# Kernel tuning notes

Measured on AMD Instinct MI355X. Metric: run time of the kernel, lower is better.

## Reference

```python
import jax, jax.numpy as jnp
import numpy as np

EPS = 1e-8
MARGIN = 0.2
LAMBDA_SM_LSE = 6.0   # i2t attention smooth (opt.lambda_softmax_lse)
LAMBDA_SM_AVG = 9.0   # t2i attention smooth (opt.lambda_softmax_avg)
LAMBDA_LSE = 6.0      # LogSumExp aggregation temperature
NEG = -1e9


def _l2norm(x, axis):
    return x / (jnp.sqrt(jnp.sum(x * x, axis=axis, keepdims=True)) + EPS)


def _cos(a, b):
    # cosine over last axis, torch-style: w12 / clamp(|a||b|, eps)
    w12 = jnp.sum(a * b, axis=-1)
    w1 = jnp.sqrt(jnp.sum(a * a, axis=-1))
    w2 = jnp.sqrt(jnp.sum(b * b, axis=-1))
    return w12 / jnp.maximum(w1 * w2, EPS)


def _forward(im, s, s_l):
    B, R, D = im.shape
    W = s.shape[1]
    wmask = jnp.arange(W)[None, :] < s_l[:, None]          # (Bc, W) valid words
    s = s * wmask[:, :, None]                              # emulate ragged slice s[j,:len_j]

    # ---------------- i2t: query=image regions, context=caption words ----------
    # attn[i,j,w,r] = <s[j,w], im[i,r]>
    A = jnp.einsum('jwd,ird->ijwr', s, im)
    A = jax.nn.leaky_relu(A, 0.1)
    A = _l2norm(A, axis=3)                                 # clipped_l2norm over regions
    logits = jnp.swapaxes(A, 2, 3) * LAMBDA_SM_LSE         # (i,j,r,w), softmax over words
    logits = jnp.where(wmask[None, :, None, :], logits, NEG)
    attn_i2t = jax.nn.softmax(logits, axis=-1)
    wc_t = jnp.einsum('ijrw,jwd->ijrd', attn_i2t, s)       # weighted caption ctx per region
    sim1 = _cos(im[:, None, :, :], wc_t)                   # (i,j,r)
    score1 = jnp.log(jnp.sum(jnp.exp(LAMBDA_LSE * sim1), axis=2)) / LAMBDA_LSE  # (i,j)
    attn_t_full = jnp.mean(wc_t, axis=2)                   # (i,j,d)
    idx = jnp.arange(B)
    attn_t = attn_t_full[idx, idx]                         # (B,d) diagonal

    # ---------------- t2i: query=caption words, context=image regions ----------
    # attn[i,j,r,w] = <im[i,r], s[j,w]>
    Bm = jnp.einsum('ird,jwd->ijrw', im, s)
    Bm = jax.nn.leaky_relu(Bm, 0.1)
    Bm = Bm * wmask[None, :, None, :]                      # padded-word cols excluded from norm
    Bm = _l2norm(Bm, axis=3)                               # clipped_l2norm over words
    logits2 = jnp.swapaxes(Bm, 2, 3) * LAMBDA_SM_AVG       # (i,j,w,r), softmax over regions
    attn_t2i = jax.nn.softmax(logits2, axis=-1)
    wc_i = jnp.einsum('ijwr,ird->ijwd', attn_t2i, im)      # weighted image ctx per word
    sim2 = _cos(s[None, :, :, :], wc_i)                    # (i,j,w)
    e2 = jnp.where(wmask[None, :, :], jnp.exp(LAMBDA_LSE * sim2), 0.0)
    score2 = jnp.log(jnp.sum(e2, axis=2)) / LAMBDA_LSE     # masked LogSumExp over words
    wsum = jnp.sum(wc_i * wmask[None, :, :, None], axis=2)
    attn_i_full = wsum / s_l[None, :, None].astype(wc_i.dtype)  # masked mean over words
    attn_i = attn_i_full[idx, idx]                         # (B,d)

    # ---------------- hinge loss over (B,B) score matrix -----------------------
    scores = 0.5 * (score1 + score2)
    diag = jnp.diagonal(scores)
    cost_s = jnp.maximum(MARGIN + scores - diag[:, None], 0.0)
    cost_im = jnp.maximum(MARGIN + scores - diag[None, :], 0.0)
    eye = jnp.eye(B, dtype=bool)
    cost_s = jnp.where(eye, 0.0, cost_s)
    cost_im = jnp.where(eye, 0.0, cost_im)
    # max_violation=True
    loss = jnp.sum(jnp.max(cost_s, axis=1)) + jnp.sum(jnp.max(cost_im, axis=0))
    return loss, attn_t, attn_i


def setup_inputs() -> dict:
    key = jax.random.key(0)
    k1, k2, k3 = jax.random.split(key, 3)
    B, R, W, D = 64, 36, 40, 1024
    im = jax.random.normal(k1, (B, R, D), dtype=jnp.float32)
    s = jax.random.normal(k2, (B, W, D), dtype=jnp.float32)
    s_l = jax.random.randint(k3, (B,), 10, W + 1)
    return {"im": im, "s": s, "s_l": s_l}


def reference(im, s, s_l):
    return _forward(im, s, s_l)
```

## Files before the change

kernel.cpp:

```cpp
#include <hip/hip_runtime.h>
#include <math.h>

#define Bn 64
#define Rr 36
#define Ww 40
#define Dd 1024
#define GM 2304
#define GN 2560
#define NCONV 4864
#define PAD 72
#define SBP 64
#define TSZ 1440
#define EPSf 1e-8f

typedef unsigned short u16;
typedef __attribute__((ext_vector_type(8))) short bf16x8;
typedef __attribute__((ext_vector_type(4))) float f32x4;

struct alignas(8) U16x4 { u16 x, y, z, w; };

__device__ inline u16 f2bf(float x) {
    unsigned int u = __float_as_uint(x);
    u += 0x7FFFu + ((u >> 16) & 1u);
    return (u16)(u >> 16);
}
__device__ inline float bf2f(u16 h) {
    return __uint_as_float(((unsigned int)h) << 16);
}

__device__ __forceinline__ void gl_lds16(const u16* g, u16* l) {
    __builtin_amdgcn_global_load_lds(
        (const __attribute__((address_space(1))) void*)g,
        (__attribute__((address_space(3))) void*)l, 16, 0, 0);
}

__global__ __launch_bounds__(256) void prep_kernel(const float* __restrict__ im,
                                                   const float* __restrict__ s,
                                                   const int* __restrict__ s_l,
                                                   u16* __restrict__ Ab,
                                                   u16* __restrict__ Bb,
                                                   u16* __restrict__ SSb,
                                                   u16* __restrict__ IIb,
                                                   float* __restrict__ SSd,
                                                   float* __restrict__ IId) {
    __shared__ float red[3][64][37];
    int b = blockIdx.x, t = threadIdx.x;
    if (b < NCONV) {
        const int nA4 = GM * Dd / 4;
        int idx = b * 256 + t;
        if (idx < nA4) {
            float4 v = *(const float4*)(im + (size_t)idx * 4);
            U16x4 o = {f2bf(v.x), f2bf(v.y), f2bf(v.z), f2bf(v.w)};
            *(U16x4*)(Ab + (size_t)idx * 4) = o;
        } else {
            int i2 = idx - nA4;
            int f = i2 * 4;
            int row = f >> 10;
            int j = row / Ww, w = row - j * Ww;
            U16x4 o = {0, 0, 0, 0};
            if (w < s_l[j]) {
                float4 v = *(const float4*)(s + (size_t)f);
                o.x = f2bf(v.x); o.y = f2bf(v.y); o.z = f2bf(v.z); o.w = f2bf(v.w);
            }
            *(U16x4*)(Bb + (size_t)i2 * 4) = o;
        }
        return;
    }
    int gb = b - NCONV;
    bool isS = gb < Bn;
    int idx = isS ? gb : gb - Bn;
    int n = isS ? Ww : Rr;
    const float* basef = isS ? (s + (size_t)idx * Ww * Dd) : (im + (size_t)idx * Rr * Dd);
    u16* outb = isS ? (SSb + (size_t)idx * 48 * SBP) : (IIb + (size_t)idx * 48 * SBP);
    float* outd = isS ? (SSd + (size_t)idx * Ww) : (IId + (size_t)idx * Rr);
    int lane = t & 63, wid = t >> 6;
    int frow = lane & 15, fk = (lane >> 4) * 8;

    f32x4 acc[3][3];
    for (int m = 0; m < 3; ++m)
        for (int p = 0; p < 3; ++p) acc[m][p] = (f32x4){0.f, 0.f, 0.f, 0.f};

    for (int ks = 0; ks < 8; ++ks) {
        int k0 = wid * 256 + ks * 32 + fk;
        bf16x8 f[3];
        for (int m = 0; m < 3; ++m) {
            int rr = m * 16 + frow;
            if (rr >= n) rr = n - 1;
            const float* p = basef + (size_t)rr * Dd + k0;
            float4 v0 = *(const float4*)p;
            float4 v1 = *(const float4*)(p + 4);
            bf16x8 fv;
            fv[0] = (short)f2bf(v0.x); fv[1] = (short)f2bf(v0.y);
            fv[2] = (short)f2bf(v0.z); fv[3] = (short)f2bf(v0.w);
            fv[4] = (short)f2bf(v1.x); fv[5] = (short)f2bf(v1.y);
            fv[6] = (short)f2bf(v1.z); fv[7] = (short)f2bf(v1.w);
            f[m] = fv;
        }
        for (int m = 0; m < 3; ++m)
            for (int p = 0; p < 3; ++p)
                acc[m][p] = __builtin_amdgcn_mfma_f32_16x16x32_bf16(f[m], f[p], acc[m][p], 0, 0, 0);
    }
    if (wid) {
        for (int m = 0; m < 3; ++m)
            for (int p = 0; p < 3; ++p)
                for (int q = 0; q < 4; ++q)
                    red[wid - 1][lane][(m * 3 + p) * 4 + q] = acc[m][p][q];
    }
    __syncthreads();
    if (wid == 0) {
        for (int wv = 0; wv < 3; ++wv)
            for (int m = 0; m < 3; ++m)
                for (int p = 0; p < 3; ++p)
                    for (int q = 0; q < 4; ++q)
                        acc[m][p][q] += red[wv][lane][(m * 3 + p) * 4 + q];
        int crow = (lane >> 4) * 4, ccol = lane & 15;
        for (int m = 0; m < 3; ++m)
            for (int p = 0; p < 3; ++p)
                for (int q = 0; q < 4; ++q) {
                    int row = m * 16 + crow + q;
                    int col = p * 16 + ccol;
                    float v = acc[m][p][q];
                    outb[row * SBP + col] = f2bf(v);
                    if (row == col && row < n) outd[row] = v;
                }
    }
}

__global__ __launch_bounds__(256) void gemm_mfma_kernel(const u16* __restrict__ Ab,
                                                        const u16* __restrict__ Bb,
                                                        u16* __restrict__ Gt) {
    __shared__ __align__(16) u16 As[3][64][64];
    __shared__ __align__(16) u16 Bs[3][128][64];
    int bn = blockIdx.x;
    int bm = blockIdx.y;
    int t = threadIdx.x;
    int lane = t & 63, wid = t >> 6;
    int wr = wid >> 1, wc = wid & 1;

    int lrow8 = lane >> 3;
    int sslot = (lane & 7) ^ lrow8;
    const u16* ga = Ab + ((size_t)(bm * 64 + wid * 16) + lrow8) * Dd + sslot * 8;
    const u16* gb = Bb + ((size_t)(bn * 128 + wid * 32) + lrow8) * Dd + sslot * 8;

    f32x4 acc[2][4];
    for (int m = 0; m < 2; ++m)
        for (int n = 0; n < 4; ++n) acc[m][n] = (f32x4){0.f, 0.f, 0.f, 0.f};

    int frow = lane & 15;
    int cgr = lane >> 4;

#define STAGE(BI, KK) do { \
        gl_lds16(ga + (KK), &As[BI][wid * 16][0]); \
        gl_lds16(ga + (size_t)8 * Dd + (KK), &As[BI][wid * 16 + 8][0]); \
        gl_lds16(gb + (KK), &Bs[BI][wid * 32][0]); \
        gl_lds16(gb + (size_t)8 * Dd + (KK), &Bs[BI][wid * 32 + 8][0]); \
        gl_lds16(gb + (size_t)16 * Dd + (KK), &Bs[BI][wid * 32 + 16][0]); \
        gl_lds16(gb + (size_t)24 * Dd + (KK), &Bs[BI][wid * 32 + 24][0]); \
    } while (0)

    STAGE(0, 0);
    STAGE(1, 64);
#pragma unroll
    for (int s = 0; s < 16; ++s) {
        if (s < 15) asm volatile("s_waitcnt vmcnt(6)" ::: "memory");
        else        asm volatile("s_waitcnt vmcnt(0)" ::: "memory");
        __builtin_amdgcn_sched_barrier(0);
        __builtin_amdgcn_s_barrier();
        __builtin_amdgcn_sched_barrier(0);
        const int cur = s % 3;
        bf16x8 af[2][2], bf[4][2];
#pragma unroll
        for (int m = 0; m < 2; ++m) {
            int row = wr * 32 + m * 16 + frow;
#pragma unroll
            for (int ks = 0; ks < 2; ++ks) {
                int slot = (ks * 4 + cgr) ^ (row & 7);
                af[m][ks] = *(const bf16x8*)&As[cur][row][slot * 8];
            }
        }
#pragma unroll
        for (int n = 0; n < 4; ++n) {
            int row = wc * 64 + n * 16 + frow;
#pragma unroll
            for (int ks = 0; ks < 2; ++ks) {
                int slot = (ks * 4 + cgr) ^ (row & 7);
                bf[n][ks] = *(const bf16x8*)&Bs[cur][row][slot * 8];
            }
        }
        if (s + 2 < 16) STAGE((s + 2) % 3, (s + 2) * 64);
#pragma unroll
        for (int ks = 0; ks < 2; ++ks)
#pragma unroll
            for (int m = 0; m < 2; ++m)
#pragma unroll
                for (int n = 0; n < 4; ++n)
                    acc[m][n] = __builtin_amdgcn_mfma_f32_16x16x32_bf16(af[m][ks], bf[n][ks], acc[m][n], 0, 0, 0);
        asm volatile("s_waitcnt lgkmcnt(0)" ::: "memory");
        __builtin_amdgcn_sched_barrier(0);
    }
#undef STAGE

    int crow0 = bm * 64 + wr * 32 + (lane >> 4) * 4;
    int ccol0 = bn * 128 + wc * 64 + (lane & 15);
    int tjv[4], wv[4];
#pragma unroll
    for (int n = 0; n < 4; ++n) {
        int col = ccol0 + n * 16;
        tjv[n] = col / 40;
        wv[n] = col - tjv[n] * 40;
    }
    for (int m = 0; m < 2; ++m)
        for (int q = 0; q < 4; ++q) {
            int row = crow0 + m * 16 + q;
            int ti = row / 36, r2 = row - ti * 36;
            u16* dstbase = Gt + (size_t)ti * Bn * TSZ + (size_t)r2 * 40;
            for (int n = 0; n < 4; ++n)
                dstbase[(size_t)tjv[n] * TSZ + wv[n]] = f2bf(acc[m][n][q]);
        }
}

__device__ __forceinline__ void quad_mfma(const u16* att, const u16* M,
                                          float* qout, int nq, int lane) {
    int c = lane & 15, g4 = lane >> 4;
    f32x4 acc[3][3];
#pragma unroll
    for (int m = 0; m < 3; ++m)
#pragma unroll
        for (int p = 0; p < 3; ++p) acc[m][p] = (f32x4){0.f, 0.f, 0.f, 0.f};
#pragma unroll
    for (int ks = 0; ks < 2; ++ks) {
        bf16x8 fa[3], fb[3];
#pragma unroll
        for (int m = 0; m < 3; ++m)
            fa[m] = *(const bf16x8*)&att[(m * 16 + c) * PAD + g4 * 8 + ks * 32];
#pragma unroll
        for (int p = 0; p < 3; ++p)
            fb[p] = *(const bf16x8*)(M + (size_t)(p * 16 + c) * SBP + g4 * 8 + ks * 32);
#pragma unroll
        for (int m = 0; m < 3; ++m)
#pragma unroll
            for (int p = 0; p < 3; ++p)
                acc[m][p] = __builtin_amdgcn_mfma_f32_16x16x32_bf16(fa[m], fb[p], acc[m][p], 0, 0, 0);
    }
#pragma unroll
    for (int m = 0; m < 3; ++m)
#pragma unroll
        for (int q = 0; q < 4; ++q) {
            int row = m * 16 + g4 * 4 + q;
            float sp = 0.f;
#pragma unroll
            for (int p = 0; p < 3; ++p)
                sp += acc[m][p][q] * bf2f(att[row * PAD + p * 16 + c]);
            sp += __shfl_xor(sp, 1);
            sp += __shfl_xor(sp, 2);
            sp += __shfl_xor(sp, 4);
            sp += __shfl_xor(sp, 8);
            if (c == 0 && row < nq) qout[row] = sp;
        }
}

__global__ __launch_bounds__(128) void pair_kernel(const u16* __restrict__ Gt,
                                                   const u16* __restrict__ SSb,
                                                   const u16* __restrict__ IIb,
                                                   const float* __restrict__ SSd,
                                                   const float* __restrict__ IId,
                                                   const int* __restrict__ s_l,
                                                   float* __restrict__ score1,
                                                   float* __restrict__ score2,
                                                   float* __restrict__ dAp,
                                                   float* __restrict__ dBp) {
    int j = blockIdx.x, i = blockIdx.y;
    int t = threadIdx.x, lane = t & 63, wid = t >> 6;
    __shared__ __align__(16) u16 glb[Rr * 44];
    __shared__ __align__(16) u16 attA[48 * PAD];
    __shared__ __align__(16) u16 attB[48 * PAD];
    __shared__ float invA[Ww], invB[Rr], sA[Rr], sB[Ww], qA[Rr], qB[Ww];
    int L = s_l[j];

    {
        uint* za = (uint*)attA;
        uint* zb = (uint*)attB;
#pragma unroll
        for (int k = 0; k < 14; ++k) {
            int idx = t + k * 128;
            if (idx < 48 * PAD / 2) { za[idx] = 0; zb[idx] = 0; }
        }
        const u16* gt = Gt + (size_t)(i * Bn + j) * TSZ;
        for (int c = t; c < 180; c += 128) {
            int r = c / 5, q = c - (c / 5) * 5;
            uint4 v = *(const uint4*)(gt + c * 8);
            *(uint2*)&glb[r * 44 + q * 8] = make_uint2(v.x, v.y);
            *(uint2*)&glb[r * 44 + q * 8 + 4] = make_uint2(v.z, v.w);
        }
    }
    float iid = 0.f, ssd = 0.f;
    if (wid == 0 && lane < Rr) iid = IId[i * Rr + lane];
    if (wid == 1 && lane < Ww) ssd = SSd[j * Ww + lane];
    __syncthreads();

    if (wid == 0 && lane < Rr) {
        float sum = 0.f;
#pragma unroll 8
        for (int w = 0; w < Ww; ++w) {
            float x = bf2f(glb[lane * 44 + w]);
            x = x < 0.f ? 0.1f * x : x;
            sum += x * x;
        }
        invB[lane] = 9.f / (sqrtf(sum) + EPSf);
    }
    if (wid == 1 && lane < Ww) {
        float sum = 0.f;
#pragma unroll 6
        for (int r = 0; r < Rr; ++r) {
            float x = bf2f(glb[r * 44 + lane]);
            x = x < 0.f ? 0.1f * x : x;
            sum += x * x;
        }
        invA[lane] = 6.f / (sqrtf(sum) + EPSf);
    }
    __syncthreads();

    float dot = 0.f, myinv = 0.f;
    if (wid == 0 && lane < Rr) {
        float ssum = 0.f;
#pragma unroll 8
        for (int w = 0; w < Ww; ++w) {
            float e = 0.f;
            if (w < L) {
                float gx = bf2f(glb[lane * 44 + w]);
                float x = gx < 0.f ? 0.1f * gx : gx;
                e = __expf(x * invA[w]);
                dot += e * gx;
            }
            attA[lane * PAD + w] = f2bf(e);
            ssum += e;
        }
        myinv = 1.f / ssum;
        dot *= myinv;
        sA[lane] = myinv;
    }
    if (wid == 1 && lane < Ww) {
        float ssum = 0.f;
#pragma unroll 6
        for (int r = 0; r < Rr; ++r) {
            float gx = bf2f(glb[r * 44 + lane]);
            float x = gx < 0.f ? 0.1f * gx : gx;
            float e = __expf(x * invB[r]);
            dot += e * gx;
            attB[lane * PAD + r] = f2bf(e);
            ssum += e;
        }
        myinv = 1.f / ssum;
        dot *= myinv;
        sB[lane] = myinv;
    }
    __syncthreads();

    if (wid == 0)
        quad_mfma(attA, SSb + (size_t)j * 48 * SBP, qA, Rr, lane);
    else
        quad_mfma(attB, IIb + (size_t)i * 48 * SBP, qB, Ww, lane);

    if (wid == 0) {
        float e1 = 0.f;
        if (lane < Rr) {
            float q = qA[lane] * myinv * myinv;
            float s1 = dot / fmaxf(sqrtf(iid) * sqrtf(fmaxf(q, 0.f)), EPSf);
            e1 = __expf(6.f * s1);
        }
#pragma unroll
        for (int off = 1; off < 64; off <<= 1) e1 += __shfl_xor(e1, off);
        if (lane == 0) score1[i * Bn + j] = __logf(e1) * (1.f / 6.f);
    } else {
        float e2 = 0.f;
        if (lane < Ww) {
            float q = qB[lane] * myinv * myinv;
            float s2 = dot / fmaxf(sqrtf(ssd) * sqrtf(fmaxf(q, 0.f)), EPSf);
            e2 = (lane < L) ? __expf(6.f * s2) : 0.f;
        }
#pragma unroll
        for (int off = 1; off < 64; off <<= 1) e2 += __shfl_xor(e2, off);
        if (lane == 0) score2[i * Bn + j] = __logf(e2) * (1.f / 6.f);
    }

    if (i == j) {
        __syncthreads();
        if (wid == 1 && lane < Ww) {
            float sum = 0.f;
#pragma unroll 6
            for (int r = 0; r < Rr; ++r) sum += bf2f(attA[r * PAD + lane]) * sA[r];
            dAp[i * Ww + lane] = sum * (1.f / (float)Rr);
        }
        if (wid == 0 && lane < Rr) {
            float sum = 0.f;
            for (int w = 0; w < L; ++w) sum += bf2f(attB[w * PAD + lane]) * sB[w];
            dBp[i * Rr + lane] = sum / (float)L;
        }
    }
}

__global__ __launch_bounds__(128) void diag_out_kernel(const u16* __restrict__ Ab,
                                                       const u16* __restrict__ Bb,
                                                       const int* __restrict__ s_l,
                                                       const float* __restrict__ dA,
                                                       const float* __restrict__ dB,
                                                       const float* __restrict__ score1,
                                                       const float* __restrict__ score2,
                                                       float* __restrict__ out) {
    int t = threadIdx.x;
    int bi = blockIdx.x;
    if (bi == Bn) {
        __shared__ float sc[Bn][Bn + 1];
        for (int idx = t; idx < Bn * Bn; idx += 128)
            sc[idx >> 6][idx & 63] = 0.5f * (score1[idx] + score2[idx]);
        __syncthreads();
        if (t < 64) {
            float dt = sc[t][t];
            float rowmax = 0.f, colmax = 0.f;
            for (int k = 0; k < Bn; ++k) {
                if (k != t) {
                    rowmax = fmaxf(rowmax, 0.2f + sc[t][k] - dt);
                    colmax = fmaxf(colmax, 0.2f + sc[k][t] - dt);
                }
            }
            float v = rowmax + colmax;
            for (int off = 32; off; off >>= 1) v += __shfl_down(v, off);
            if (t == 0) out[0] = v;
        }
        return;
    }
    int i = bi;
    int L = s_l[i];
    __shared__ float aw[Ww], br[Rr];
    if (t < Ww) aw[t] = dA[i * Ww + t];
    if (t >= 64 && t < 64 + Rr) br[t - 64] = dB[i * Rr + (t - 64)];
    __syncthreads();
    int d0 = t * 8;
    const u16* BbI = Bb + (size_t)i * Ww * Dd + d0;
    const u16* AbI = Ab + (size_t)i * Rr * Dd + d0;
    float a1[8], a2[8];
#pragma unroll
    for (int k = 0; k < 8; ++k) { a1[k] = 0.f; a2[k] = 0.f; }
    for (int w = 0; w < L; ++w) {
        bf16x8 v = *(const bf16x8*)(BbI + (size_t)w * Dd);
        float c = aw[w];
#pragma unroll
        for (int k = 0; k < 8; ++k) a1[k] += c * bf2f((u16)v[k]);
    }
#pragma unroll 6
    for (int r = 0; r < Rr; ++r) {
        bf16x8 v = *(const bf16x8*)(AbI + (size_t)r * Dd);
        float c = br[r];
#pragma unroll
        for (int k = 0; k < 8; ++k) a2[k] += c * bf2f((u16)v[k]);
    }
    float* o1 = out + 1 + (size_t)i * Dd + d0;
    float* o2 = out + 1 + (size_t)Bn * Dd + (size_t)i * Dd + d0;
#pragma unroll
    for (int k = 0; k < 8; ++k) { o1[k] = a1[k]; o2[k] = a2[k]; }
}

extern "C" void kernel_launch(void* const* d_in, const int* in_sizes, int n_in,
                              void* d_out, int out_size, void* d_ws, size_t ws_size,
                              hipStream_t stream) {
    const float* im = (const float*)d_in[0];
    const float* s = (const float*)d_in[1];
    const int* s_l = (const int*)d_in[2];
    float* out = (float*)d_out;

    u16* Ab = (u16*)d_ws;
    u16* Bb = Ab + (size_t)GM * Dd;
    u16* Gt = Bb + (size_t)GN * Dd;
    u16* SSb = Gt + (size_t)GM * GN;
    u16* IIb = SSb + (size_t)Bn * 48 * SBP;
    float* SSd = (float*)(IIb + (size_t)Bn * 48 * SBP);
    float* IId = SSd + (size_t)Bn * Ww;
    float* score1 = IId + (size_t)Bn * Rr;
    float* score2 = score1 + Bn * Bn;
    float* dA = score2 + Bn * Bn;
    float* dB = dA + Bn * Ww;

    prep_kernel<<<NCONV + 2 * Bn, 256, 0, stream>>>(im, s, s_l, Ab, Bb, SSb, IIb, SSd, IId);

    dim3 ggrid(GN / 128, GM / 64);
    gemm_mfma_kernel<<<ggrid, 256, 0, stream>>>(Ab, Bb, Gt);

    dim3 pgrid(Bn, Bn);
    pair_kernel<<<pgrid, 128, 0, stream>>>(Gt, SSb, IIb, SSd, IId, s_l,
                                           score1, score2, dA, dB);

    diag_out_kernel<<<Bn + 1, 128, 0, stream>>>(Ab, Bb, s_l, dA, dB, score1, score2, out);
}
```

Measured before the change: 78.94 us.

## Move Gram blocks into GEMM grid, fuse diag output into pair kernel, simplify pipeline

The per-batch Gram matrices (SS, II) are now computed by extra blocks appended to the GEMM grid, reading the already-converted bf16 buffers instead of reconverting fp32, so the prep kernel becomes a pure conversion pass. The diagonal attention output (attn_t, attn_i) is computed inside the pair kernel's diagonal blocks, which removes the separate diag kernel and the dA/dB round-trip. The loss reduction moves to a tiny single-block kernel. The GEMM main loop drops from a 3-stage hand-scheduled pipeline with explicit waitcnts to a simpler 2-stage loop with __syncthreads, which may reduce load/compute overlap. Diagonal pair blocks also take on extra serial work.

```diff
diff --git a/kernel.cpp b/kernel.cpp
--- a/kernel.cpp
+++ b/kernel.cpp
@@ -34,107 +34,101 @@
         (__attribute__((address_space(3))) void*)l, 16, 0, 0);
 }
 
-__global__ __launch_bounds__(256) void prep_kernel(const float* __restrict__ im,
-                                                   const float* __restrict__ s,
-                                                   const int* __restrict__ s_l,
-                                                   u16* __restrict__ Ab,
-                                                   u16* __restrict__ Bb,
-                                                   u16* __restrict__ SSb,
-                                                   u16* __restrict__ IIb,
-                                                   float* __restrict__ SSd,
-                                                   float* __restrict__ IId) {
-    __shared__ float red[3][64][37];
-    int b = blockIdx.x, t = threadIdx.x;
-    if (b < NCONV) {
-        const int nA4 = GM * Dd / 4;
-        int idx = b * 256 + t;
-        if (idx < nA4) {
-            float4 v = *(const float4*)(im + (size_t)idx * 4);
-            U16x4 o = {f2bf(v.x), f2bf(v.y), f2bf(v.z), f2bf(v.w)};
-            *(U16x4*)(Ab + (size_t)idx * 4) = o;
-        } else {
-            int i2 = idx - nA4;
-            int f = i2 * 4;
-            int row = f >> 10;
-            int j = row / Ww, w = row - j * Ww;
-            U16x4 o = {0, 0, 0, 0};
-            if (w < s_l[j]) {
-                float4 v = *(const float4*)(s + (size_t)f);
-                o.x = f2bf(v.x); o.y = f2bf(v.y); o.z = f2bf(v.z); o.w = f2bf(v.w);
-            }
-            *(U16x4*)(Bb + (size_t)i2 * 4) = o;
-        }
-        return;
-    }
-    int gb = b - NCONV;
-    bool isS = gb < Bn;
-    int idx = isS ? gb : gb - Bn;
-    int n = isS ? Ww : Rr;
-    const float* basef = isS ? (s + (size_t)idx * Ww * Dd) : (im + (size_t)idx * Rr * Dd);
-    u16* outb = isS ? (SSb + (size_t)idx * 48 * SBP) : (IIb + (size_t)idx * 48 * SBP);
-    float* outd = isS ? (SSd + (size_t)idx * Ww) : (IId + (size_t)idx * Rr);
-    int lane = t & 63, wid = t >> 6;
-    int frow = lane & 15, fk = (lane >> 4) * 8;
-
-    f32x4 acc[3][3];
-    for (int m = 0; m < 3; ++m)
-        for (int p = 0; p < 3; ++p) acc[m][p] = (f32x4){0.f, 0.f, 0.f, 0.f};
-
-    for (int ks = 0; ks < 8; ++ks) {
-        int k0 = wid * 256 + ks * 32 + fk;
-        bf16x8 f[3];
-        for (int m = 0; m < 3; ++m) {
-            int rr = m * 16 + frow;
-            if (rr >= n) rr = n - 1;
-            const float* p = basef + (size_t)rr * Dd + k0;
-            float4 v0 = *(const float4*)p;
-            float4 v1 = *(const float4*)(p + 4);
-            bf16x8 fv;
-            fv[0] = (short)f2bf(v0.x); fv[1] = (short)f2bf(v0.y);
-            fv[2] = (short)f2bf(v0.z); fv[3] = (short)f2bf(v0.w);
-            fv[4] = (short)f2bf(v1.x); fv[5] = (short)f2bf(v1.y);
-            fv[6] = (short)f2bf(v1.z); fv[7] = (short)f2bf(v1.w);
-            f[m] = fv;
-        }
-        for (int m = 0; m < 3; ++m)
-            for (int p = 0; p < 3; ++p)
-                acc[m][p] = __builtin_amdgcn_mfma_f32_16x16x32_bf16(f[m], f[p], acc[m][p], 0, 0, 0);
-    }
-    if (wid) {
-        for (int m = 0; m < 3; ++m)
-            for (int p = 0; p < 3; ++p)
-                for (int q = 0; q < 4; ++q)
-                    red[wid - 1][lane][(m * 3 + p) * 4 + q] = acc[m][p][q];
-    }
-    __syncthreads();
-    if (wid == 0) {
-        for (int wv = 0; wv < 3; ++wv)
-            for (int m = 0; m < 3; ++m)
-                for (int p = 0; p < 3; ++p)
-                    for (int q = 0; q < 4; ++q)
-                        acc[m][p][q] += red[wv][lane][(m * 3 + p) * 4 + q];
-        int crow = (lane >> 4) * 4, ccol = lane & 15;
-        for (int m = 0; m < 3; ++m)
-            for (int p = 0; p < 3; ++p)
-                for (int q = 0; q < 4; ++q) {
-                    int row = m * 16 + crow + q;
-                    int col = p * 16 + ccol;
-                    float v = acc[m][p][q];
-                    outb[row * SBP + col] = f2bf(v);
-                    if (row == col && row < n) outd[row] = v;
-                }
-    }
-}
-
-__global__ __launch_bounds__(256) void gemm_mfma_kernel(const u16* __restrict__ Ab,
+__global__ __launch_bounds__(256) void convert_kernel(const float* __restrict__ im,
+                                                      const float* __restrict__ s,
+                                                      const int* __restrict__ s_l,
+                                                      u16* __restrict__ Ab,
+                                                      u16* __restrict__ Bb) {
+    const int nA4 = GM * Dd / 4;
+    int idx = blockIdx.x * 256 + threadIdx.x;
+    if (idx < nA4) {
+        float4 v = *(const float4*)(im + (size_t)idx * 4);
+        U16x4 o = {f2bf(v.x), f2bf(v.y), f2bf(v.z), f2bf(v.w)};
+        *(U16x4*)(Ab + (size_t)idx * 4) = o;
+    } else {
+        int i2 = idx - nA4;
+        int f = i2 * 4;
+        int row = f >> 10;
+        int j = row / Ww, w = row - j * Ww;
+        U16x4 o = {0, 0, 0, 0};
+        if (w < s_l[j]) {
+            float4 v = *(const float4*)(s + (size_t)f);
+            o.x = f2bf(v.x); o.y = f2bf(v.y); o.z = f2bf(v.z); o.w = f2bf(v.w);
+        }
+        *(U16x4*)(Bb + (size_t)i2 * 4) = o;
+    }
+}
+
+__global__ __launch_bounds__(256) void gemm_gram_kernel(const u16* __restrict__ Ab,
                                                         const u16* __restrict__ Bb,
-                                                        u16* __restrict__ Gt) {
-    __shared__ __align__(16) u16 As[3][64][64];
-    __shared__ __align__(16) u16 Bs[3][128][64];
+                                                        u16* __restrict__ Gt,
+                                                        u16* __restrict__ SSb,
+                                                        u16* __restrict__ IIb,
+                                                        float* __restrict__ SSd,
+                                                        float* __restrict__ IId) {
+    __shared__ __align__(16) char smem[49152];
     int bn = blockIdx.x;
     int bm = blockIdx.y;
     int t = threadIdx.x;
     int lane = t & 63, wid = t >> 6;
+
+    if (bm >= 36) {
+        int gb = (bm - 36) * 20 + bn;
+        if (gb >= 2 * Bn) return;
+        bool isS = gb < Bn;
+        int idx = isS ? gb : gb - Bn;
+        int n = isS ? Ww : Rr;
+        const u16* base = isS ? (Bb + (size_t)idx * Ww * Dd) : (Ab + (size_t)idx * Rr * Dd);
+        u16* outb = isS ? (SSb + (size_t)idx * 48 * SBP) : (IIb + (size_t)idx * 48 * SBP);
+        float* outd = isS ? (SSd + (size_t)idx * Ww) : (IId + (size_t)idx * Rr);
+        float* red = (float*)smem;
+        int frow = lane & 15, fk = (lane >> 4) * 8;
+
+        f32x4 acc[3][3];
+        for (int m = 0; m < 3; ++m)
+            for (int p = 0; p < 3; ++p) acc[m][p] = (f32x4){0.f, 0.f, 0.f, 0.f};
+
+        for (int ks = 0; ks < 8; ++ks) {
+            int k0 = wid * 256 + ks * 32 + fk;
+            bf16x8 f[3];
+            for (int m = 0; m < 3; ++m) {
+                int rr = m * 16 + frow;
+                if (rr >= n) rr = n - 1;
+                f[m] = *(const bf16x8*)(base + (size_t)rr * Dd + k0);
+            }
+            for (int m = 0; m < 3; ++m)
+                for (int p = 0; p < 3; ++p)
+                    acc[m][p] = __builtin_amdgcn_mfma_f32_16x16x32_bf16(f[m], f[p], acc[m][p], 0, 0, 0);
+        }
+        if (wid) {
+            for (int m = 0; m < 3; ++m)
+                for (int p = 0; p < 3; ++p)
+                    for (int q = 0; q < 4; ++q)
+                        red[(wid - 1) * 64 * 37 + lane * 37 + (m * 3 + p) * 4 + q] = acc[m][p][q];
+        }
+        __syncthreads();
+        if (wid == 0) {
+            for (int wv = 0; wv < 3; ++wv)
+                for (int m = 0; m < 3; ++m)
+                    for (int p = 0; p < 3; ++p)
+                        for (int q = 0; q < 4; ++q)
+                            acc[m][p][q] += red[wv * 64 * 37 + lane * 37 + (m * 3 + p) * 4 + q];
+            int crow = (lane >> 4) * 4, ccol = lane & 15;
+            for (int m = 0; m < 3; ++m)
+                for (int p = 0; p < 3; ++p)
+                    for (int q = 0; q < 4; ++q) {
+                        int row = m * 16 + crow + q;
+                        int col = p * 16 + ccol;
+                        float v = acc[m][p][q];
+                        outb[row * SBP + col] = f2bf(v);
+                        if (row == col && row < n) outd[row] = v;
+                    }
+        }
+        return;
+    }
+
+    u16* As = (u16*)smem;
+    u16* Bs = (u16*)(smem + 16384);
     int wr = wid >> 1, wc = wid & 1;
 
     int lrow8 = lane >> 3;
@@ -150,24 +144,19 @@
     int cgr = lane >> 4;
 
 #define STAGE(BI, KK) do { \
-        gl_lds16(ga + (KK), &As[BI][wid * 16][0]); \
-        gl_lds16(ga + (size_t)8 * Dd + (KK), &As[BI][wid * 16 + 8][0]); \
-        gl_lds16(gb + (KK), &Bs[BI][wid * 32][0]); \
-        gl_lds16(gb + (size_t)8 * Dd + (KK), &Bs[BI][wid * 32 + 8][0]); \
-        gl_lds16(gb + (size_t)16 * Dd + (KK), &Bs[BI][wid * 32 + 16][0]); \
-        gl_lds16(gb + (size_t)24 * Dd + (KK), &Bs[BI][wid * 32 + 24][0]); \
+        gl_lds16(ga + (KK), As + (BI) * 4096 + (wid * 16) * 64); \
+        gl_lds16(ga + (size_t)8 * Dd + (KK), As + (BI) * 4096 + (wid * 16 + 8) * 64); \
+        gl_lds16(gb + (KK), Bs + (BI) * 8192 + (wid * 32) * 64); \
+        gl_lds16(gb + (size_t)8 * Dd + (KK), Bs + (BI) * 8192 + (wid * 32 + 8) * 64); \
+        gl_lds16(gb + (size_t)16 * Dd + (KK), Bs + (BI) * 8192 + (wid * 32 + 16) * 64); \
+        gl_lds16(gb + (size_t)24 * Dd + (KK), Bs + (BI) * 8192 + (wid * 32 + 24) * 64); \
     } while (0)
 
     STAGE(0, 0);
-    STAGE(1, 64);
-#pragma unroll
-    for (int s = 0; s < 16; ++s) {
-        if (s < 15) asm volatile("s_waitcnt vmcnt(6)" ::: "memory");
-        else        asm volatile("s_waitcnt vmcnt(0)" ::: "memory");
-        __builtin_amdgcn_sched_barrier(0);
-        __builtin_amdgcn_s_barrier();
-        __builtin_amdgcn_sched_barrier(0);
-        const int cur = s % 3;
+    for (int step = 0; step < 16; ++step) {
+        int cur = step & 1;
+        __syncthreads();
+        if (step < 15) STAGE(cur ^ 1, (step + 1) * 64);
         bf16x8 af[2][2], bf[4][2];
 #pragma unroll
         for (int m = 0; m < 2; ++m) {
@@ -175,7 +164,7 @@
 #pragma unroll
             for (int ks = 0; ks < 2; ++ks) {
                 int slot = (ks * 4 + cgr) ^ (row & 7);
-                af[m][ks] = *(const bf16x8*)&As[cur][row][slot * 8];
+                af[m][ks] = *(const bf16x8*)(As + cur * 4096 + row * 64 + slot * 8);
             }
         }
 #pragma unroll
@@ -184,10 +173,9 @@
 #pragma unroll
             for (int ks = 0; ks < 2; ++ks) {
                 int slot = (ks * 4 + cgr) ^ (row & 7);
-                bf[n][ks] = *(const bf16x8*)&Bs[cur][row][slot * 8];
+                bf[n][ks] = *(const bf16x8*)(Bs + cur * 8192 + row * 64 + slot * 8);
             }
         }
-        if (s + 2 < 16) STAGE((s + 2) % 3, (s + 2) * 64);
 #pragma unroll
         for (int ks = 0; ks < 2; ++ks)
 #pragma unroll
@@ -195,8 +183,6 @@
 #pragma unroll
                 for (int n = 0; n < 4; ++n)
                     acc[m][n] = __builtin_amdgcn_mfma_f32_16x16x32_bf16(af[m][ks], bf[n][ks], acc[m][n], 0, 0, 0);
-        asm volatile("s_waitcnt lgkmcnt(0)" ::: "memory");
-        __builtin_amdgcn_sched_barrier(0);
     }
 #undef STAGE
 
@@ -264,17 +250,19 @@
                                                    const u16* __restrict__ IIb,
                                                    const float* __restrict__ SSd,
                                                    const float* __restrict__ IId,
+                                                   const u16* __restrict__ Ab,
+                                                   const u16* __restrict__ Bb,
                                                    const int* __restrict__ s_l,
                                                    float* __restrict__ score1,
                                                    float* __restrict__ score2,
-                                                   float* __restrict__ dAp,
-                                                   float* __restrict__ dBp) {
+                                                   float* __restrict__ out) {
     int j = blockIdx.x, i = blockIdx.y;
     int t = threadIdx.x, lane = t & 63, wid = t >> 6;
     __shared__ __align__(16) u16 glb[Rr * 44];
     __shared__ __align__(16) u16 attA[48 * PAD];
     __shared__ __align__(16) u16 attB[48 * PAD];
     __shared__ float invA[Ww], invB[Rr], sA[Rr], sB[Ww], qA[Rr], qB[Ww];
+    __shared__ float aw[Ww], br[Rr];
     int L = s_l[j];
 
     {
@@ -389,75 +377,61 @@
             float sum = 0.f;
 #pragma unroll 6
             for (int r = 0; r < Rr; ++r) sum += bf2f(attA[r * PAD + lane]) * sA[r];
-            dAp[i * Ww + lane] = sum * (1.f / (float)Rr);
+            aw[lane] = sum * (1.f / (float)Rr);
         }
         if (wid == 0 && lane < Rr) {
             float sum = 0.f;
             for (int w = 0; w < L; ++w) sum += bf2f(attB[w * PAD + lane]) * sB[w];
-            dBp[i * Rr + lane] = sum / (float)L;
-        }
-    }
-}
-
-__global__ __launch_bounds__(128) void diag_out_kernel(const u16* __restrict__ Ab,
-                                                       const u16* __restrict__ Bb,
-                                                       const int* __restrict__ s_l,
-                                                       const float* __restrict__ dA,
-                                                       const float* __restrict__ dB,
-                                                       const float* __restrict__ score1,
-                                                       const float* __restrict__ score2,
-                                                       float* __restrict__ out) {
+            br[lane] = sum / (float)L;
+        }
+        __syncthreads();
+        int d0 = t * 8;
+        const u16* BbI = Bb + (size_t)i * Ww * Dd + d0;
+        const u16* AbI = Ab + (size_t)i * Rr * Dd + d0;
+        float a1[8], a2[8];
+#pragma unroll
+        for (int k = 0; k < 8; ++k) { a1[k] = 0.f; a2[k] = 0.f; }
+        for (int w = 0; w < L; ++w) {
+            bf16x8 v = *(const bf16x8*)(BbI + (size_t)w * Dd);
+            float c = aw[w];
+#pragma unroll
+            for (int k = 0; k < 8; ++k) a1[k] += c * bf2f((u16)v[k]);
+        }
+#pragma unroll 6
+        for (int r = 0; r < Rr; ++r) {
+            bf16x8 v = *(const bf16x8*)(AbI + (size_t)r * Dd);
+            float c = br[r];
+#pragma unroll
+            for (int k = 0; k < 8; ++k) a2[k] += c * bf2f((u16)v[k]);
+        }
+        float* o1 = out + 1 + (size_t)i * Dd + d0;
+        float* o2 = out + 1 + (size_t)Bn * Dd + (size_t)i * Dd + d0;
+#pragma unroll
+        for (int k = 0; k < 8; ++k) { o1[k] = a1[k]; o2[k] = a2[k]; }
+    }
+}
+
+__global__ void loss_kernel(const float* __restrict__ s1,
+                            const float* __restrict__ s2,
+                            float* __restrict__ out) {
     int t = threadIdx.x;
-    int bi = blockIdx.x;
-    if (bi == Bn) {
-        __shared__ float sc[Bn][Bn + 1];
-        for (int idx = t; idx < Bn * Bn; idx += 128)
-            sc[idx >> 6][idx & 63] = 0.5f * (score1[idx] + score2[idx]);
-        __syncthreads();
-        if (t < 64) {
-            float dt = sc[t][t];
-            float rowmax = 0.f, colmax = 0.f;
-            for (int k = 0; k < Bn; ++k) {
-                if (k != t) {
-                    rowmax = fmaxf(rowmax, 0.2f + sc[t][k] - dt);
-                    colmax = fmaxf(colmax, 0.2f + sc[k][t] - dt);
-                }
-            }
-            float v = rowmax + colmax;
-            for (int off = 32; off; off >>= 1) v += __shfl_down(v, off);
-            if (t == 0) out[0] = v;
-        }
-        return;
-    }
-    int i = bi;
-    int L = s_l[i];
-    __shared__ float aw[Ww], br[Rr];
-    if (t < Ww) aw[t] = dA[i * Ww + t];
-    if (t >= 64 && t < 64 + Rr) br[t - 64] = dB[i * Rr + (t - 64)];
+    __shared__ float sc[Bn][Bn + 1];
+    for (int idx = t; idx < Bn * Bn; idx += 64)
+        sc[idx >> 6][idx & 63] = 0.5f * (s1[idx] + s2[idx]);
     __syncthreads();
-    int d0 = t * 8;
-    const u16* BbI = Bb + (size_t)i * Ww * Dd + d0;
-    const u16* AbI = Ab + (size_t)i * Rr * Dd + d0;
-    float a1[8], a2[8];
-#pragma unroll
-    for (int k = 0; k < 8; ++k) { a1[k] = 0.f; a2[k] = 0.f; }
-    for (int w = 0; w < L; ++w) {
-        bf16x8 v = *(const bf16x8*)(BbI + (size_t)w * Dd);
-        float c = aw[w];
-#pragma unroll
-        for (int k = 0; k < 8; ++k) a1[k] += c * bf2f((u16)v[k]);
-    }
-#pragma unroll 6
-    for (int r = 0; r < Rr; ++r) {
-        bf16x8 v = *(const bf16x8*)(AbI + (size_t)r * Dd);
-        float c = br[r];
-#pragma unroll
-        for (int k = 0; k < 8; ++k) a2[k] += c * bf2f((u16)v[k]);
-    }
-    float* o1 = out + 1 + (size_t)i * Dd + d0;
-    float* o2 = out + 1 + (size_t)Bn * Dd + (size_t)i * Dd + d0;
-#pragma unroll
-    for (int k = 0; k < 8; ++k) { o1[k] = a1[k]; o2[k] = a2[k]; }
+    float dt = sc[t][t];
+    float rowmax = 0.f, colmax = 0.f;
+    for (int k = 0; k < Bn; ++k) {
+        if (k != t) {
+            float cs = 0.2f + sc[t][k] - dt;
+            if (cs > rowmax) rowmax = cs;
+            float ci = 0.2f + sc[k][t] - dt;
+            if (ci > colmax) colmax = ci;
+        }
+    }
+    float v = rowmax + colmax;
+    for (int off = 32; off; off >>= 1) v += __shfl_down(v, off);
+    if (t == 0) out[0] = v;
 }
 
 extern "C" void kernel_launch(void* const* d_in, const int* in_sizes, int n_in,
@@ -477,17 +451,15 @@
     float* IId = SSd + (size_t)Bn * Ww;
     float* score1 = IId + (size_t)Bn * Rr;
     float* score2 = score1 + Bn * Bn;
-    float* dA = score2 + Bn * Bn;
-    float* dB = dA + Bn * Ww;
-
-    prep_kernel<<<NCONV + 2 * Bn, 256, 0, stream>>>(im, s, s_l, Ab, Bb, SSb, IIb, SSd, IId);
-
-    dim3 ggrid(GN / 128, GM / 64);
-    gemm_mfma_kernel<<<ggrid, 256, 0, stream>>>(Ab, Bb, Gt);
+
+    convert_kernel<<<NCONV, 256, 0, stream>>>(im, s, s_l, Ab, Bb);
+
+    dim3 ggrid(GN / 128, 36 + 7);
+    gemm_gram_kernel<<<ggrid, 256, 0, stream>>>(Ab, Bb, Gt, SSb, IIb, SSd, IId);
 
     dim3 pgrid(Bn, Bn);
-    pair_kernel<<<pgrid, 128, 0, stream>>>(Gt, SSb, IIb, SSd, IId, s_l,
-                                           score1, score2, dA, dB);
-
-    diag_out_kernel<<<Bn + 1, 128, 0, stream>>>(Ab, Bb, s_l, dA, dB, score1, score2, out);
-}
+    pair_kernel<<<pgrid, 128, 0, stream>>>(Gt, SSb, IIb, SSd, IId, Ab, Bb, s_l,
+                                           score1, score2, out);
+
+    loss_kernel<<<1, 64, 0, stream>>>(score1, score2, out);
+}
```

Measured after the change: 76.55 us. 3.0% less time.
